# Performance work log

Measured on AMD Instinct MI355X. Metric: run time of the kernel, lower is better.

The kernel has to match this reference:

```python
import jax, jax.numpy as jnp
import numpy as np
from jax import lax

B, L, V = 128, 64, 8192
E = H = 128
STEPS = 10
MAX_BIN = 512
BETA_START, BETA_END = 1e-4, 2e-2


def setup_inputs():
    key = jax.random.key(0)
    k = jax.random.split(key, 23)
    s = 0.05
    padded_x = (jax.random.uniform(k[0], (B, L, V)) < 0.01).astype(jnp.float32)
    lengths = jax.random.randint(k[1], (B,), 1, L + 1)
    visit_mask = (jnp.arange(L)[None, :] < lengths[:, None]).astype(jnp.float32)
    padded_bins = jnp.sort(jax.random.randint(k[2], (B, L), 0, MAX_BIN), axis=1)
    t_diff = jax.random.randint(k[3], (B,), 1, STEPS + 1)
    eps = jax.random.normal(k[4], (B, L, E))
    z0 = jax.random.normal(k[5], (B, L, E))
    noise = jax.random.normal(k[6], (STEPS, B, L, E))
    W_visit = jax.random.normal(k[7], (E, V)) * s
    bin_embed = (jax.random.normal(k[8], (MAX_BIN + 2, E)) * s).at[0].set(0.0)  # padding_idx=0
    W_ih = jax.random.normal(k[9], (4 * H, E)) * s
    W_hh = jax.random.normal(k[10], (4 * H, H)) * s
    b_ih = jax.random.normal(k[11], (4 * H,)) * s
    b_hh = jax.random.normal(k[12], (4 * H,)) * s
    W_cls = jax.random.normal(k[13], (1, H)) * s
    b_cls = jax.random.normal(k[14], (1,)) * s
    W_proj = jax.random.normal(k[15], (E, H)) * s
    time_embed = jax.random.normal(k[16], (STEPS + 1, E)) * s
    W_fuse = jax.random.normal(k[17], (2, 2 * E)) * s
    b_fuse = jax.random.normal(k[18], (2,)) * s
    W_e1 = jax.random.normal(k[19], (E, 2 * E)) * s
    b_e1 = jax.random.normal(k[20], (E,)) * s
    W_e2 = jax.random.normal(k[21], (E, E)) * s
    b_e2 = jax.random.normal(k[22], (E,)) * s
    return dict(padded_x=padded_x, visit_mask=visit_mask, padded_bins=padded_bins,
                t_diff=t_diff, eps=eps, z0=z0, noise=noise, W_visit=W_visit,
                bin_embed=bin_embed, W_ih=W_ih, W_hh=W_hh, b_ih=b_ih, b_hh=b_hh,
                W_cls=W_cls, b_cls=b_cls, W_proj=W_proj, time_embed=time_embed,
                W_fuse=W_fuse, b_fuse=b_fuse, W_e1=W_e1, b_e1=b_e1, W_e2=W_e2, b_e2=b_e2)


def _lstm(v, W_ih, W_hh, b_ih, b_hh):
    # v: [B,L,E] -> h: [B,L,H]; PyTorch gate order i,f,g,o
    xg = jnp.einsum('ble,ge->blg', v, W_ih) + b_ih + b_hh
    def step(carry, x):
        h, c = carry
        g = x + h @ W_hh.T
        i, f, gg, o = jnp.split(g, 4, axis=-1)
        c = jax.nn.sigmoid(f) * c + jax.nn.sigmoid(i) * jnp.tanh(gg)
        h = jax.nn.sigmoid(o) * jnp.tanh(c)
        return (h, c), h
    z = jnp.zeros((v.shape[0], W_hh.shape[1]), v.dtype)
    _, hs = lax.scan(step, (z, z), jnp.swapaxes(xg, 0, 1))
    return jnp.swapaxes(hs, 0, 1)


def _last_hidden(h, mask):
    lengths = jnp.maximum(mask.sum(axis=1).astype(jnp.int32), 1)
    return h[jnp.arange(h.shape[0]), lengths - 1]


def reference(padded_x, visit_mask, padded_bins, t_diff, eps, z0, noise,
              W_visit, bin_embed, W_ih, W_hh, b_ih, b_hh, W_cls, b_cls,
              W_proj, time_embed, W_fuse, b_fuse, W_e1, b_e1, W_e2, b_e2):
    m = visit_mask[..., None]                      # [B,L,1]
    betas = jnp.linspace(BETA_START, BETA_END, STEPS)
    alphas = 1.0 - betas
    alpha_bars = jnp.cumprod(alphas)

    # visit embedding + time-gap (delta bin) embedding
    delta = jnp.concatenate([jnp.zeros_like(padded_bins[:, :1]),
                             jnp.clip(padded_bins[:, 1:] - padded_bins[:, :-1], 0)], axis=1)
    delta = jnp.where(visit_mask > 0, jnp.clip(delta, 0, MAX_BIN + 1), 0)
    v = (padded_x @ W_visit.T + bin_embed[delta]) * m  # [B,L,E]

    # encoder LSTM (packed seq == plain scan then zero padded suffix positions)
    h = _lstm(v, W_ih, W_hh, b_ih, b_hh) * m
    logits_real = (_last_hidden(h, visit_mask) @ W_cls.T + b_cls)[:, 0]

    h_prev = jnp.pad(h[:, :-1], ((0, 0), (1, 0), (0, 0)))
    hp = (h_prev @ W_proj.T) * m                   # [B,L,E]

    def fuse_eps(z, t_emb):
        a = jax.nn.softmax(jnp.concatenate([z, hp], -1) @ W_fuse.T + b_fuse, axis=-1)
        g = a[..., :1] * z + a[..., 1:] * hp
        x = jnp.concatenate([g, t_emb], -1)
        return jax.nn.relu(x @ W_e1.T + b_e1) @ W_e2.T + b_e2

    # diffusion loss
    t = jnp.where(visit_mask > 0, t_diff[:, None], 1)    # [B,L]
    ab = alpha_bars[t - 1][..., None]
    z_t = (jnp.sqrt(ab) * v + jnp.sqrt(1.0 - ab) * eps) * m
    eps_pred = fuse_eps(z_t, time_embed[t])
    denom = jnp.maximum(visit_mask.sum(), 1.0)
    diffusion_loss = jnp.sum((eps_pred - eps) ** 2 * m) / denom

    # reverse diffusion sampling of synthetic visit embeddings
    def step(z, inp):
        kk, nz = inp
        t_s = jnp.where(visit_mask > 0, kk, 1)
        e = fuse_eps(z, time_embed[t_s])
        beta = betas[kk - 1]
        mean = (z - beta / jnp.sqrt(1.0 - alpha_bars[kk - 1]) * e) / jnp.sqrt(alphas[kk - 1])
        z = jnp.where(kk > 1, mean + jnp.sqrt(beta) * nz, mean) * m
        return z, None

    ks = jnp.arange(STEPS, 0, -1)
    v_syn, _ = lax.scan(step, z0, (ks, noise))

    h_syn = _lstm(v_syn, W_ih, W_hh, b_ih, b_hh) * m
    logits_syn = (_last_hidden(h_syn, visit_mask) @ W_cls.T + b_cls)[:, 0]
    return logits_real, logits_syn, diffusion_loss
```

## Files before the change

kernel.cpp:

```cpp
#include <hip/hip_runtime.h>

#define B_ 128
#define L_ 64
#define V_ 8192
#define E_ 128
#define H_ 128
#define NROW (B_*L_)
#define HSTRIDE 136
#define AS 136
#define XS 264
#define YS 136
#define ZS 132
#define HS2 136

typedef unsigned short u16;
typedef __attribute__((ext_vector_type(8))) short bf16x8;
typedef __attribute__((ext_vector_type(4))) float f32x4;

__device__ __forceinline__ float sigm(float x){ return 1.f/(1.f + __expf(-x)); }
__device__ __forceinline__ float ftanh(float x){ float e = __expf(2.f*x); return 1.f - 2.f/(e + 1.f); }
__device__ __forceinline__ u16 f2bf(float f){
    union { unsigned int i; float f; } x; x.f = f;
    unsigned int r = x.i + 0x7fff + ((x.i >> 16) & 1);
    return (u16)(r >> 16);
}
#define LBAR() asm volatile("s_waitcnt lgkmcnt(0)\ns_barrier" ::: "memory")

__device__ __forceinline__ bf16x8 pack8(const float* p){
    const float4* q = (const float4*)p;
    float4 a = q[0], b = q[1];
    bf16x8 f;
    f[0]=(short)f2bf(a.x); f[1]=(short)f2bf(a.y); f[2]=(short)f2bf(a.z); f[3]=(short)f2bf(a.w);
    f[4]=(short)f2bf(b.x); f[5]=(short)f2bf(b.y); f[6]=(short)f2bf(b.z); f[7]=(short)f2bf(b.w);
    return f;
}

__global__ __launch_bounds__(256) void k_prep(const float* __restrict__ Wv, float* __restrict__ WT,
                                              const float* __restrict__ Whh, const float* __restrict__ Wih,
                                              const float* __restrict__ We1, const float* __restrict__ We2,
                                              const float* __restrict__ Wproj,
                                              u16* __restrict__ dWhh, u16* __restrict__ dWih,
                                              u16* __restrict__ dWe1, u16* __restrict__ dWe2,
                                              u16* __restrict__ dWproj){
    __shared__ float tile[16][129];
    int t = threadIdx.x;
    if(blockIdx.x < 512){
        int v0 = blockIdx.x * 16;
        #pragma unroll
        for(int i=0;i<8;i++){
            int idx = i*256 + t; int e = idx >> 4; int vv = idx & 15;
            tile[vv][e] = Wv[(size_t)e*V_ + v0 + vv];
        }
        __syncthreads();
        #pragma unroll
        for(int i=0;i<8;i++){
            int idx = i*256 + t; int vv = idx >> 7; int e = idx & 127;
            WT[(size_t)(v0+vv)*E_ + e] = tile[vv][e];
        }
        return;
    }
    int bid = blockIdx.x - 512;
    const float* src; u16* dst; int WS,TS,NT,KT,K; int base;
    if(bid<32){ src=Whh; dst=dWhh; WS=16; TS=128; NT=4; KT=4; K=128; base=bid; }
    else if(bid<64){ src=Wih; dst=dWih; WS=128; TS=16; NT=8; KT=4; K=128; base=bid-32; }
    else if(bid<80){ src=We1; dst=dWe1; WS=32; TS=16; NT=2; KT=8; K=256; base=bid-64; }
    else if(bid<88){ src=We2; dst=dWe2; WS=32; TS=16; NT=2; KT=4; K=128; base=bid-80; }
    else { src=Wproj; dst=dWproj; WS=32; TS=16; NT=2; KT=4; K=128; base=bid-88; }
    for(int i=0;i<8;i++){
        int o = base*2048 + i*256 + t;
        int g = o >> 9; int lane = (o >> 3) & 63; int j = o & 7;
        int kt = g % KT; int r2 = g / KT; int nt = r2 % NT; int w = r2 / NT;
        int lc = lane & 15; int quad = lane >> 4;
        int n = w*WS + nt*TS + lc; int k = kt*32 + quad*8 + j;
        dst[o] = f2bf(src[(size_t)n*K + k]);
    }
}

__global__ __launch_bounds__(256) void k_visit_embed(const float* __restrict__ px, const float* __restrict__ vmask,
                                                     const int* __restrict__ bins, const float* __restrict__ bemb,
                                                     const float* __restrict__ WT, float* __restrict__ v){
    __shared__ int idxs[512];
    __shared__ int cnt;
    __shared__ int dsh;
    __shared__ float msh;
    __shared__ float4 red[8][32];
    int row = blockIdx.x; int l = row & 63;
    int t = threadIdx.x;
    if(t==0){
        cnt = 0;
        float m = vmask[row];
        int d = 0;
        if(l > 0){ d = bins[row] - bins[row-1]; d = d < 0 ? 0 : (d > 513 ? 513 : d); }
        if(!(m > 0.f)) d = 0;
        dsh = d; msh = m;
    }
    __syncthreads();
    const uint4* xr4 = (const uint4*)(px + (size_t)row * V_);
    uint4 u8[8];
    #pragma unroll
    for(int i=0;i<8;i++) u8[i] = xr4[t + i*256];
    #pragma unroll
    for(int i=0;i<8;i++){
        unsigned int w[4] = {u8[i].x,u8[i].y,u8[i].z,u8[i].w};
        #pragma unroll
        for(int j=0;j<4;j++){
            if(w[j]){ int p = atomicAdd(&cnt,1); if(p<512) idxs[p] = (t + i*256)*4 + j; }
        }
    }
    __syncthreads();
    int n = cnt; if(n > 512) n = 512;
    int eq = t & 31, jg = t >> 5;
    float4 a4 = {0.f,0.f,0.f,0.f};
    for(int j=jg;j<n;j+=8){
        const float4* wr = (const float4*)(WT + (size_t)idxs[j]*E_);
        float4 wv = wr[eq];
        a4.x += wv.x; a4.y += wv.y; a4.z += wv.z; a4.w += wv.w;
    }
    red[jg][eq] = a4;
    __syncthreads();
    if(t < 32){
        float4 s = red[0][t];
        #pragma unroll
        for(int g=1;g<8;g++){
            float4 r = red[g][t];
            s.x += r.x; s.y += r.y; s.z += r.z; s.w += r.w;
        }
        const float4* bp = (const float4*)(bemb + dsh*E_);
        float4 bv = bp[t];
        float m = msh;
        float4 o;
        o.x = (s.x + bv.x)*m; o.y = (s.y + bv.y)*m; o.z = (s.z + bv.z)*m; o.w = (s.w + bv.w)*m;
        ((float4*)(v + (size_t)row*E_))[t] = o;
    }
}

__global__ __launch_bounds__(256,2) void k_gemm_xgp(const float* __restrict__ A, const u16* __restrict__ Wihp,
                                                    const float* __restrict__ bih, const float* __restrict__ bhh,
                                                    float* __restrict__ xgp){
    __shared__ __align__(16) u16 abuf[2][16*AS];
    int t = threadIdx.x, wave = t >> 6, lane = t & 63, quad = lane >> 4, lc = lane & 15;
    int bid = blockIdx.x; int bg = bid >> 5, l0 = (bid & 31)*2;
    #pragma unroll
    for(int i=0;i<16;i++){
        int flat = i*256 + t; int s = flat >> 11; int r = (flat >> 7) & 15; int e = flat & 127;
        abuf[s][r*AS + e] = f2bf(A[((size_t)(bg*16+r)*64 + l0 + s)*E_ + e]);
    }
    bf16x8 wg[8][4]; float bb[8];
    #pragma unroll
    for(int nt=0;nt<8;nt++){
        int n = wave*128 + nt*16 + lc;
        bb[nt] = bih[n] + bhh[n];
        #pragma unroll
        for(int kt=0;kt<4;kt++)
            wg[nt][kt] = *(const bf16x8*)(Wihp + (((wave*8+nt)*4+kt)<<9) + lane*8);
    }
    __syncthreads();
    #pragma unroll
    for(int s=0;s<2;s++){
        f32x4 ac[8];
        #pragma unroll
        for(int nt=0;nt<8;nt++) ac[nt] = (f32x4){0.f,0.f,0.f,0.f};
        #pragma unroll
        for(int kt=0;kt<4;kt++){
            bf16x8 af = *(const bf16x8*)&abuf[s][lc*AS + kt*32 + quad*8];
            #pragma unroll
            for(int nt=0;nt<8;nt++)
                ac[nt] = __builtin_amdgcn_mfma_f32_16x16x32_bf16(af, wg[nt][kt], ac[nt], 0,0,0);
        }
        float* dst = xgp + (size_t)(bg*64 + l0 + s)*8192;
        #pragma unroll
        for(int nt=0;nt<8;nt++){
            float4 o;
            o.x = ac[nt][0] + bb[nt]; o.y = ac[nt][1] + bb[nt];
            o.z = ac[nt][2] + bb[nt]; o.w = ac[nt][3] + bb[nt];
            *(float4*)(dst + nt*1024 + quad*256 + lc*16 + wave*4) = o;
        }
    }
}

template<bool STOREH>
__device__ __forceinline__ void lstm_step(int l,
        const u16* __restrict__ bufr, u16* __restrict__ bufw,
        const f32x4*& pxg, u16* hsp,
        const bf16x8 (&bfh)[4][4],
        f32x4 (&xc)[4], f32x4 (&xn)[4], float (&c4)[4], float (&lg4)[4],
        const int (&len4)[4], float wcv, int lc, int quad, int cw){
    if(l+1 < 64){
        #pragma unroll
        for(int g=0;g<4;g++) xn[g] = pxg[g];
        pxg += 2048;
    }
    bf16x8 afh[4];
    #pragma unroll
    for(int kt=0;kt<4;kt++)
        afh[kt] = *(const bf16x8*)&bufr[lc*HSTRIDE + kt*32 + quad*8];
    f32x4 acc[4];
    #pragma unroll
    for(int g=0;g<4;g++) acc[g] = (f32x4){0.f,0.f,0.f,0.f};
    #pragma unroll
    for(int kt=0;kt<4;kt++){
        #pragma unroll
        for(int g=0;g<4;g++)
            acc[g] = __builtin_amdgcn_mfma_f32_16x16x32_bf16(afh[kt], bfh[g][kt], acc[g], 0,0,0);
    }
    #pragma unroll
    for(int r=0;r<4;r++){
        float gi = acc[0][r] + xc[0][r];
        float gf = acc[1][r] + xc[1][r];
        float gg = acc[2][r] + xc[2][r];
        float go = acc[3][r] + xc[3][r];
        float c  = sigm(gf)*c4[r] + sigm(gi)*ftanh(gg);
        float h  = sigm(go)*ftanh(c);
        c4[r] = c;
        u16 hb = f2bf(h);
        bufw[(quad*4+r)*HSTRIDE + cw] = hb;
        if constexpr (STOREH) hsp[(size_t)r*8192 + (size_t)l*128] = hb;
        if(l == len4[r]-1) lg4[r] += h * wcv;
    }
    LBAR();
}

template<bool STOREH>
__global__ __attribute__((amdgpu_waves_per_eu(2,2))) __launch_bounds__(512)
void k_lstm(const float* __restrict__ xgp, const u16* __restrict__ Whhp,
            const float* __restrict__ Wcls, const float* __restrict__ bcls,
            const float* __restrict__ vmask, u16* __restrict__ h_store,
            float* __restrict__ logits_out){
    __shared__ __align__(16) u16 hbuf[2][16*HSTRIDE];
    __shared__ float vmsh[16*64];
    __shared__ int lensh[16];
    __shared__ float lgsh[16][132];
    int t = threadIdx.x;
    int wave = t >> 6, lane = t & 63;
    int quad = lane >> 4, lc = lane & 15;
    int cw = wave*16 + lc;
    int bg = blockIdx.x; int b0 = bg * 16;

    for(int i=t;i<16*HSTRIDE;i+=512) hbuf[0][i] = 0;
    for(int i=t;i<1024;i+=512) vmsh[i] = vmask[b0*64 + i];
    __syncthreads();
    if(t < 16){
        int s = 0;
        #pragma unroll
        for(int i=0;i<64;i++) s += (vmsh[t*64 + i] > 0.f) ? 1 : 0;
        lensh[t] = s < 1 ? 1 : s;
    }

    bf16x8 bfh[4][4];
    #pragma unroll
    for(int g=0;g<4;g++)
        #pragma unroll
        for(int kt=0;kt<4;kt++)
            bfh[g][kt] = *(const bf16x8*)(Whhp + (((wave*4+g)*4+kt)<<9) + lane*8);
    float wcv = Wcls[cw];
    float c4[4] = {0.f,0.f,0.f,0.f};
    float lg4[4] = {0.f,0.f,0.f,0.f};
    u16* hsp = STOREH ? (h_store + ((size_t)(b0 + quad*4)*64)*128 + cw) : (u16*)nullptr;

    const f32x4* pxg = (const f32x4*)(xgp + (size_t)bg*64*8192) + t*4;
    f32x4 x0[4], x1[4];
    #pragma unroll
    for(int g=0;g<4;g++) x0[g] = pxg[g];
    pxg += 2048;
    __syncthreads();
    int len4[4];
    #pragma unroll
    for(int r=0;r<4;r++) len4[r] = lensh[quad*4 + r];

    for(int lb=0;lb<64;lb+=2){
        lstm_step<STOREH>(lb,   hbuf[0], hbuf[1], pxg, hsp, bfh, x0, x1, c4, lg4, len4, wcv, lc, quad, cw);
        lstm_step<STOREH>(lb+1, hbuf[1], hbuf[0], pxg, hsp, bfh, x1, x0, c4, lg4, len4, wcv, lc, quad, cw);
    }
    #pragma unroll
    for(int r=0;r<4;r++) lgsh[quad*4+r][cw] = lg4[r];
    __syncthreads();
    {
        int row = t >> 5, l32 = t & 31;
        float s = lgsh[row][l32] + lgsh[row][l32+32] + lgsh[row][l32+64] + lgsh[row][l32+96];
        s += __shfl_down(s, 16, 32);
        s += __shfl_down(s, 8, 32);
        s += __shfl_down(s, 4, 32);
        s += __shfl_down(s, 2, 32);
        s += __shfl_down(s, 1, 32);
        if(l32 == 0) logits_out[b0 + row] = s + bcls[0];
    }
}

__global__ __launch_bounds__(256,2) void k_drg(const float* __restrict__ v, const u16* __restrict__ h,
        const float* __restrict__ eps, const int* __restrict__ tdiff, const float* __restrict__ vmask,
        const float* __restrict__ z0, const float* __restrict__ noise, const float* __restrict__ temb,
        const float* __restrict__ Wf, const float* __restrict__ bfu,
        const u16* __restrict__ We1p, const float* __restrict__ be1,
        const u16* __restrict__ We2p, const float* __restrict__ be2,
        const u16* __restrict__ Wprojp,
        float* __restrict__ partial, float* __restrict__ vsyn){
    __shared__ __align__(16) float zbuf[16*ZS];
    __shared__ float hpbuf[16*ZS];
    __shared__ __align__(16) u16 xbuf[16*XS];
    __shared__ __align__(16) u16 y1buf[16*YS];
    __shared__ __align__(16) u16 hb16[16*HS2];
    __shared__ float wfsh[512];
    __shared__ float ssh[16][2], hpd[16][2];
    __shared__ float mrow[16]; __shared__ int trow[16];
    __shared__ float sbeta[10], sabar[10];
    __shared__ float rb[4];
    int row0 = blockIdx.x * 16; int t = threadIdx.x;
    int wave = t >> 6, lane = t & 63, quad = lane >> 4, lc = lane & 15;

    if(t==0){
        float p = 1.f;
        for(int k=0;k<10;k++){ float b = 1e-4f + (0.02f - 1e-4f)*k/9.f; sbeta[k] = b; p *= (1.f - b); sabar[k] = p; }
    }
    if(t < 16){
        int row = row0 + t; float m = vmask[row];
        mrow[t] = m; trow[t] = (m > 0.f) ? tdiff[row >> 6] : 1;
    }
    for(int i=t;i<512;i+=256) wfsh[i] = Wf[i];
    __syncthreads();
    #pragma unroll
    for(int i=0;i<8;i++){
        int flat = i*256 + t; int r = flat >> 7; int e = flat & 127; int row = row0 + r;
        float ab = sabar[trow[r]-1];
        zbuf[r*ZS + e] = (sqrtf(ab)*v[(size_t)row*E_ + e] + sqrtf(1.f - ab)*eps[(size_t)row*E_ + e]) * mrow[r];
    }
    {
        int r = t >> 4, e0 = (t & 15) * 8;
        bf16x8 hv;
        if(((row0 & 63) == 0) && r == 0){
            hv = (bf16x8){0,0,0,0,0,0,0,0};
        } else {
            hv = *(const bf16x8*)(h + (size_t)(row0 - 1 + r)*E_ + e0);
        }
        *(bf16x8*)&hb16[r*HS2 + e0] = hv;
    }
    bf16x8 wf1[2][8], wf2[2][4], pf[2][4];
    float be1v[2], be2v[2];
    #pragma unroll
    for(int nt=0;nt<2;nt++){
        int n = wave*32 + nt*16 + lc;
        be1v[nt] = be1[n]; be2v[nt] = be2[n];
        #pragma unroll
        for(int kt=0;kt<8;kt++) wf1[nt][kt] = *(const bf16x8*)(We1p + (((wave*2+nt)*8+kt)<<9) + lane*8);
        #pragma unroll
        for(int kt=0;kt<4;kt++){
            wf2[nt][kt] = *(const bf16x8*)(We2p + (((wave*2+nt)*4+kt)<<9) + lane*8);
            pf[nt][kt]  = *(const bf16x8*)(Wprojp + (((wave*2+nt)*4+kt)<<9) + lane*8);
        }
    }
    __syncthreads();
    {
        f32x4 ap[2];
        ap[0] = (f32x4){0.f,0.f,0.f,0.f}; ap[1] = (f32x4){0.f,0.f,0.f,0.f};
        #pragma unroll
        for(int kt=0;kt<4;kt++){
            bf16x8 af = *(const bf16x8*)&hb16[lc*HS2 + kt*32 + quad*8];
            ap[0] = __builtin_amdgcn_mfma_f32_16x16x32_bf16(af, pf[0][kt], ap[0], 0,0,0);
            ap[1] = __builtin_amdgcn_mfma_f32_16x16x32_bf16(af, pf[1][kt], ap[1], 0,0,0);
        }
        #pragma unroll
        for(int nt=0;nt<2;nt++)
            #pragma unroll
            for(int rr=0;rr<4;rr++)
                hpbuf[(quad*4+rr)*ZS + wave*32 + nt*16 + lc] = ap[nt][rr];
    }
    __syncthreads();
    {
        int row = t >> 4, k = (t >> 3) & 1, sub = t & 7;
        float p = 0.f;
        #pragma unroll
        for(int i=0;i<16;i++)
            p += hpbuf[row*ZS + sub*16 + i] * wfsh[k*256 + 128 + sub*16 + i];
        p += __shfl_down(p,4); p += __shfl_down(p,2); p += __shfl_down(p,1);
        if(sub == 0) hpd[row][k] = p + bfu[k];
    }
    __syncthreads();

    for(int s=0;s<11;s++){
        int kk = 11 - s;
        float nzv[8], epv[8], z0v[8];
        if(s >= 1){
            #pragma unroll
            for(int nt=0;nt<2;nt++)
                #pragma unroll
                for(int r=0;r<4;r++)
                    nzv[nt*4+r] = noise[((size_t)(s-1)*NROW + row0 + quad*4 + r)*E_ + wave*32 + nt*16 + lc];
        } else {
            #pragma unroll
            for(int nt=0;nt<2;nt++)
                #pragma unroll
                for(int r=0;r<4;r++)
                    epv[nt*4+r] = eps[(size_t)(row0 + quad*4 + r)*E_ + wave*32 + nt*16 + lc];
            #pragma unroll
            for(int i=0;i<8;i++){
                int flat = i*256 + t;
                z0v[i] = z0[(size_t)(row0 + (flat >> 7))*E_ + (flat & 127)];
            }
        }
        {
            int row = t >> 4, k = (t >> 3) & 1, sub = t & 7;
            float q = 0.f;
            #pragma unroll
            for(int i=0;i<16;i++)
                q += zbuf[row*ZS + sub*16 + i] * wfsh[k*256 + sub*16 + i];
            q += __shfl_down(q,4); q += __shfl_down(q,2); q += __shfl_down(q,1);
            if(sub == 0) ssh[row][k] = q + hpd[row][k];
        }
        __syncthreads();
        {
            int row = t >> 4, c0 = (t & 15) * 16;
            float s0 = ssh[row][0], s1 = ssh[row][1];
            float a0 = 1.f/(1.f + __expf(s1 - s0)), a1 = 1.f - a0;
            int tt = (s == 0) ? trow[row] : ((mrow[row] > 0.f) ? kk : 1);
            #pragma unroll
            for(int i=0;i<16;i++){
                int c = c0 + i;
                float val = (c < 128) ? (a0*zbuf[row*ZS + c] + a1*hpbuf[row*ZS + c])
                                      : temb[tt*E_ + (c - 128)];
                xbuf[row*XS + c] = f2bf(val);
            }
        }
        __syncthreads();
        f32x4 acc1[2];
        acc1[0] = (f32x4){0.f,0.f,0.f,0.f}; acc1[1] = (f32x4){0.f,0.f,0.f,0.f};
        #pragma unroll
        for(int kt=0;kt<8;kt++){
            bf16x8 af = *(const bf16x8*)&xbuf[lc*XS + kt*32 + quad*8];
            acc1[0] = __builtin_amdgcn_mfma_f32_16x16x32_bf16(af, wf1[0][kt], acc1[0], 0,0,0);
            acc1[1] = __builtin_amdgcn_mfma_f32_16x16x32_bf16(af, wf1[1][kt], acc1[1], 0,0,0);
        }
        #pragma unroll
        for(int nt=0;nt<2;nt++){
            #pragma unroll
            for(int r=0;r<4;r++)
                y1buf[(quad*4+r)*YS + wave*32 + nt*16 + lc] = f2bf(fmaxf(acc1[nt][r] + be1v[nt], 0.f));
        }
        __syncthreads();
        f32x4 acc2[2];
        acc2[0] = (f32x4){0.f,0.f,0.f,0.f}; acc2[1] = (f32x4){0.f,0.f,0.f,0.f};
        #pragma unroll
        for(int kt=0;kt<4;kt++){
            bf16x8 af = *(const bf16x8*)&y1buf[lc*YS + kt*32 + quad*8];
            acc2[0] = __builtin_amdgcn_mfma_f32_16x16x32_bf16(af, wf2[0][kt], acc2[0], 0,0,0);
            acc2[1] = __builtin_amdgcn_mfma_f32_16x16x32_bf16(af, wf2[1][kt], acc2[1], 0,0,0);
        }
        if(s == 0){
            float lp = 0.f;
            #pragma unroll
            for(int nt=0;nt<2;nt++){
                #pragma unroll
                for(int r=0;r<4;r++){
                    int m = quad*4 + r;
                    float d = (acc2[nt][r] + be2v[nt]) - epv[nt*4+r];
                    lp += d*d*mrow[m];
                }
            }
            #pragma unroll
            for(int off=32;off;off>>=1) lp += __shfl_down(lp, off);
            if(lane == 0) rb[wave] = lp;
            __syncthreads();
            if(t == 0) partial[blockIdx.x] = rb[0]+rb[1]+rb[2]+rb[3];
            #pragma unroll
            for(int i=0;i<8;i++){
                int flat = i*256 + t; int r = flat >> 7; int e = flat & 127;
                zbuf[r*ZS + e] = z0v[i];
            }
            __syncthreads();
        } else {
            float beta = sbeta[kk-1];
            float c1 = beta / sqrtf(1.f - sabar[kk-1]);
            float c2 = 1.f / sqrtf(1.f - beta);
            float sb = sqrtf(beta);
            #pragma unroll
            for(int nt=0;nt<2;nt++){
                int n = wave*32 + nt*16 + lc;
                #pragma unroll
                for(int r=0;r<4;r++){
                    int m = quad*4 + r;
                    float e = acc2[nt][r] + be2v[nt];
                    float z = zbuf[m*ZS + n];
                    float mean = (z - c1*e) * c2;
                    float nz = nzv[nt*4+r];
                    float znew = (kk > 1) ? (mean + sb*nz) : mean;
                    zbuf[m*ZS + n] = znew * mrow[m];
                }
            }
            __syncthreads();
        }
    }
    {
        int r = t >> 4, e0 = (t & 15) * 8;
        float4 a = *(const float4*)&zbuf[r*ZS + e0];
        float4 b2 = *(const float4*)&zbuf[r*ZS + e0 + 4];
        *(float4*)&vsyn[(size_t)(row0 + r)*E_ + e0] = a;
        *(float4*)&vsyn[(size_t)(row0 + r)*E_ + e0 + 4] = b2;
    }
}

__global__ void k_finalize(const float* __restrict__ partial, const float* __restrict__ vmask, float* __restrict__ out){
    __shared__ float rb[4], rl[4];
    int t = threadIdx.x;
    float s = 0.f;
    for(int i=t;i<NROW;i+=256) s += vmask[i];
    float ls = 0.f;
    for(int i=t;i<512;i+=256) ls += partial[i];
    #pragma unroll
    for(int off=32;off;off>>=1){ s += __shfl_down(s, off); ls += __shfl_down(ls, off); }
    if((t & 63) == 0){ rb[t >> 6] = s; rl[t >> 6] = ls; }
    __syncthreads();
    if(t == 0){
        float denom = rb[0]+rb[1]+rb[2]+rb[3];
        if(denom < 1.f) denom = 1.f;
        out[256] = (rl[0]+rl[1]+rl[2]+rl[3]) / denom;
    }
}

extern "C" void kernel_launch(void* const* d_in, const int* in_sizes, int n_in,
                              void* d_out, int out_size, void* d_ws, size_t ws_size,
                              hipStream_t stream){
    const float* px    = (const float*)d_in[0];
    const float* vmask = (const float*)d_in[1];
    const int*   bins  = (const int*)d_in[2];
    const int*   tdiff = (const int*)d_in[3];
    const float* eps   = (const float*)d_in[4];
    const float* z0    = (const float*)d_in[5];
    const float* noise = (const float*)d_in[6];
    const float* Wv    = (const float*)d_in[7];
    const float* bemb  = (const float*)d_in[8];
    const float* Wih   = (const float*)d_in[9];
    const float* Whh   = (const float*)d_in[10];
    const float* bih   = (const float*)d_in[11];
    const float* bhh   = (const float*)d_in[12];
    const float* Wcls  = (const float*)d_in[13];
    const float* bcls  = (const float*)d_in[14];
    const float* Wproj = (const float*)d_in[15];
    const float* temb  = (const float*)d_in[16];
    const float* Wf    = (const float*)d_in[17];
    const float* bfu   = (const float*)d_in[18];
    const float* We1   = (const float*)d_in[19];
    const float* be1   = (const float*)d_in[20];
    const float* We2   = (const float*)d_in[21];
    const float* be2   = (const float*)d_in[22];
    float* out = (float*)d_out;

    float* ws = (float*)d_ws;
    float* xgp     = ws;
    float* WT      = ws + 4194304;
    float* v       = ws + 5242880;
    float* vsyn    = ws + 6291456;
    float* partial = ws + 7340032;
    u16*  Whh_p    = (u16*)(ws + 7340544);
    u16*  Wih_p    = Whh_p + 65536;
    u16*  We1_p    = Whh_p + 131072;
    u16*  We2_p    = Whh_p + 163840;
    u16*  Wproj_p  = Whh_p + 180224;
    u16*  h_store  = (u16*)(ws + 7438848);

    hipLaunchKernelGGL(k_prep, dim3(608), dim3(256), 0, stream, Wv, WT,
                       Whh, Wih, We1, We2, Wproj, Whh_p, Wih_p, We1_p, We2_p, Wproj_p);
    hipLaunchKernelGGL(k_visit_embed, dim3(NROW), dim3(256), 0, stream, px, vmask, bins, bemb, WT, v);
    hipLaunchKernelGGL(k_gemm_xgp, dim3(256), dim3(256), 0, stream, v, Wih_p, bih, bhh, xgp);
    hipLaunchKernelGGL((k_lstm<true>), dim3(B_/16), dim3(512), 0, stream,
                       xgp, Whh_p, Wcls, bcls, vmask, h_store, out);
    hipLaunchKernelGGL(k_drg, dim3(NROW/16), dim3(256), 0, stream,
                       v, h_store, eps, tdiff, vmask, z0, noise, temb, Wf, bfu,
                       We1_p, be1, We2_p, be2, Wproj_p, partial, vsyn);
    hipLaunchKernelGGL(k_gemm_xgp, dim3(256), dim3(256), 0, stream, vsyn, Wih_p, bih, bhh, xgp);
    hipLaunchKernelGGL((k_lstm<false>), dim3(B_/16), dim3(512), 0, stream,
                       xgp, Whh_p, Wcls, bcls, vmask, (u16*)nullptr, out + 128);
    hipLaunchKernelGGL(k_finalize, dim3(1), dim3(256), 0, stream, partial, vmask, out);
}
```

Measured before the change: 725.4 us.

## Fuse input-gate GEMM into diffusion kernel and finalize into second LSTM

The reverse-diffusion kernel now projects its final synthetic embeddings through W_ih with MFMA and writes gate pre-activations straight into the layout the LSTM expects. This removes the v_syn round trip and one GEMM launch. The diffusion-loss finalize reduction moves into block 0 of the second LSTM kernel, removing another launch. The cost is extra registers and weight loads in k_drg, plus serial tail work in one LSTM block.

Result: no change. 732.2 us (+0.9%).

```diff
diff --git a/kernel.cpp b/kernel.cpp
--- a/kernel.cpp
+++ b/kernel.cpp
@@ -25,15 +25,6 @@
     return (u16)(r >> 16);
 }
 #define LBAR() asm volatile("s_waitcnt lgkmcnt(0)\ns_barrier" ::: "memory")
-
-__device__ __forceinline__ bf16x8 pack8(const float* p){
-    const float4* q = (const float4*)p;
-    float4 a = q[0], b = q[1];
-    bf16x8 f;
-    f[0]=(short)f2bf(a.x); f[1]=(short)f2bf(a.y); f[2]=(short)f2bf(a.z); f[3]=(short)f2bf(a.w);
-    f[4]=(short)f2bf(b.x); f[5]=(short)f2bf(b.y); f[6]=(short)f2bf(b.z); f[7]=(short)f2bf(b.w);
-    return f;
-}
 
 __global__ __launch_bounds__(256) void k_prep(const float* __restrict__ Wv, float* __restrict__ WT,
                                               const float* __restrict__ Whh, const float* __restrict__ Wih,
@@ -225,7 +216,7 @@
 void k_lstm(const float* __restrict__ xgp, const u16* __restrict__ Whhp,
             const float* __restrict__ Wcls, const float* __restrict__ bcls,
             const float* __restrict__ vmask, u16* __restrict__ h_store,
-            float* __restrict__ logits_out){
+            const float* __restrict__ partial, float* __restrict__ logits_out){
     __shared__ __align__(16) u16 hbuf[2][16*HSTRIDE];
     __shared__ float vmsh[16*64];
     __shared__ int lensh[16];
@@ -284,6 +275,25 @@
         s += __shfl_down(s, 1, 32);
         if(l32 == 0) logits_out[b0 + row] = s + bcls[0];
     }
+    if constexpr (!STOREH){
+        if(bg == 0){
+            __syncthreads();
+            float s = 0.f;
+            for(int i=t;i<NROW;i+=512) s += vmask[i];
+            float ls = partial[t];
+            #pragma unroll
+            for(int off=32;off;off>>=1){ s += __shfl_down(s, off); ls += __shfl_down(ls, off); }
+            if(lane == 0){ lgsh[0][wave] = s; lgsh[1][wave] = ls; }
+            __syncthreads();
+            if(t == 0){
+                float sd = 0.f, lt = 0.f;
+                #pragma unroll
+                for(int w=0;w<8;w++){ sd += lgsh[0][w]; lt += lgsh[1][w]; }
+                if(sd < 1.f) sd = 1.f;
+                logits_out[128] = lt / sd;
+            }
+        }
+    }
 }
 
 __global__ __launch_bounds__(256,2) void k_drg(const float* __restrict__ v, const u16* __restrict__ h,
@@ -292,8 +302,9 @@
         const float* __restrict__ Wf, const float* __restrict__ bfu,
         const u16* __restrict__ We1p, const float* __restrict__ be1,
         const u16* __restrict__ We2p, const float* __restrict__ be2,
-        const u16* __restrict__ Wprojp,
-        float* __restrict__ partial, float* __restrict__ vsyn){
+        const u16* __restrict__ Wprojp, const u16* __restrict__ Wihp,
+        const float* __restrict__ bih, const float* __restrict__ bhh,
+        float* __restrict__ partial, float* __restrict__ xgp){
     __shared__ __align__(16) float zbuf[16*ZS];
     __shared__ float hpbuf[16*ZS];
     __shared__ __align__(16) u16 xbuf[16*XS];
@@ -489,28 +500,39 @@
     }
     {
         int r = t >> 4, e0 = (t & 15) * 8;
-        float4 a = *(const float4*)&zbuf[r*ZS + e0];
-        float4 b2 = *(const float4*)&zbuf[r*ZS + e0 + 4];
-        *(float4*)&vsyn[(size_t)(row0 + r)*E_ + e0] = a;
-        *(float4*)&vsyn[(size_t)(row0 + r)*E_ + e0 + 4] = b2;
-    }
-}
-
-__global__ void k_finalize(const float* __restrict__ partial, const float* __restrict__ vmask, float* __restrict__ out){
-    __shared__ float rb[4], rl[4];
-    int t = threadIdx.x;
-    float s = 0.f;
-    for(int i=t;i<NROW;i+=256) s += vmask[i];
-    float ls = 0.f;
-    for(int i=t;i<512;i+=256) ls += partial[i];
-    #pragma unroll
-    for(int off=32;off;off>>=1){ s += __shfl_down(s, off); ls += __shfl_down(ls, off); }
-    if((t & 63) == 0){ rb[t >> 6] = s; rl[t >> 6] = ls; }
-    __syncthreads();
-    if(t == 0){
-        float denom = rb[0]+rb[1]+rb[2]+rb[3];
-        if(denom < 1.f) denom = 1.f;
-        out[256] = (rl[0]+rl[1]+rl[2]+rl[3]) / denom;
+        #pragma unroll
+        for(int i=0;i<8;i++)
+            xbuf[r*XS + e0 + i] = f2bf(zbuf[r*ZS + e0 + i]);
+    }
+    __syncthreads();
+    {
+        bf16x8 wg[8][4]; float bb[8];
+        #pragma unroll
+        for(int nt=0;nt<8;nt++){
+            int n = wave*128 + nt*16 + lc;
+            bb[nt] = bih[n] + bhh[n];
+            #pragma unroll
+            for(int kt=0;kt<4;kt++)
+                wg[nt][kt] = *(const bf16x8*)(Wihp + (((wave*8+nt)*4+kt)<<9) + lane*8);
+        }
+        f32x4 ac[8];
+        #pragma unroll
+        for(int nt=0;nt<8;nt++) ac[nt] = (f32x4){0.f,0.f,0.f,0.f};
+        #pragma unroll
+        for(int kt=0;kt<4;kt++){
+            bf16x8 af = *(const bf16x8*)&xbuf[lc*XS + kt*32 + quad*8];
+            #pragma unroll
+            for(int nt=0;nt<8;nt++)
+                ac[nt] = __builtin_amdgcn_mfma_f32_16x16x32_bf16(af, wg[nt][kt], ac[nt], 0,0,0);
+        }
+        int b = row0 >> 6; int bg = b >> 4; int rrb = b & 15; int l0 = row0 & 63;
+        float* base = xgp + (size_t)(bg*64 + l0)*8192 + (rrb>>2)*256 + (rrb&3);
+        #pragma unroll
+        for(int nt=0;nt<8;nt++){
+            #pragma unroll
+            for(int r=0;r<4;r++)
+                base[(size_t)(quad*4 + r)*8192 + nt*1024 + lc*16 + wave*4] = ac[nt][r] + bb[nt];
+        }
     }
 }
 
@@ -546,7 +568,6 @@
     float* xgp     = ws;
     float* WT      = ws + 4194304;
     float* v       = ws + 5242880;
-    float* vsyn    = ws + 6291456;
     float* partial = ws + 7340032;
     u16*  Whh_p    = (u16*)(ws + 7340544);
     u16*  Wih_p    = Whh_p + 65536;
@@ -560,12 +581,10 @@
     hipLaunchKernelGGL(k_visit_embed, dim3(NROW), dim3(256), 0, stream, px, vmask, bins, bemb, WT, v);
     hipLaunchKernelGGL(k_gemm_xgp, dim3(256), dim3(256), 0, stream, v, Wih_p, bih, bhh, xgp);
     hipLaunchKernelGGL((k_lstm<true>), dim3(B_/16), dim3(512), 0, stream,
-                       xgp, Whh_p, Wcls, bcls, vmask, h_store, out);
+                       xgp, Whh_p, Wcls, bcls, vmask, h_store, (const float*)nullptr, out);
     hipLaunchKernelGGL(k_drg, dim3(NROW/16), dim3(256), 0, stream,
                        v, h_store, eps, tdiff, vmask, z0, noise, temb, Wf, bfu,
-                       We1_p, be1, We2_p, be2, Wproj_p, partial, vsyn);
-    hipLaunchKernelGGL(k_gemm_xgp, dim3(256), dim3(256), 0, stream, vsyn, Wih_p, bih, bhh, xgp);
+                       We1_p, be1, We2_p, be2, Wproj_p, Wih_p, bih, bhh, partial, xgp);
     hipLaunchKernelGGL((k_lstm<false>), dim3(B_/16), dim3(512), 0, stream,
-                       xgp, Whh_p, Wcls, bcls, vmask, (u16*)nullptr, out + 128);
-    hipLaunchKernelGGL(k_finalize, dim3(1), dim3(256), 0, stream, partial, vmask, out);
-}
+                       xgp, Whh_p, Wcls, bcls, vmask, (u16*)nullptr, partial, out + 128);
+}
```
